# Kernel tuning notes

Measured on AMD Instinct MI355X. Metric: run time of the kernel, lower is better.

Reference implementation:

```python
import jax, jax.numpy as jnp
import numpy as np
from jax import lax


def _pairwise_dist(a, b):
    # a: (T, D), b: (T, D) -> (T, T) Euclidean distances via GEMM trick
    a2 = jnp.sum(a * a, axis=-1)
    b2 = jnp.sum(b * b, axis=-1)
    sq = a2[:, None] + b2[None, :] - 2.0 * (a @ b.T)
    return jnp.sqrt(jnp.maximum(sq, 1e-12))


def _frechet(seq1, seq2):
    cost = _pairwise_dist(seq1, seq2)  # (T, T)
    ca0 = lax.cummax(cost[0])          # first row boundary: running max

    def row_step(prev, cost_row):
        # prev: ca[i-1, :]; cost_row: cost[i, :]
        c0 = jnp.maximum(prev[0], cost_row[0])  # first-column boundary

        def col_step(left, x):
            c, up, diag = x
            val = jnp.maximum(c, jnp.minimum(jnp.minimum(up, left), diag))
            return val, val

        _, rest = lax.scan(col_step, c0, (cost_row[1:], prev[1:], prev[:-1]))
        cur = jnp.concatenate([c0[None], rest])
        return cur, None

    final_row, _ = lax.scan(row_step, ca0, cost[1:])
    return final_row[-1]


def setup_inputs() -> dict:
    key = jax.random.key(0)
    k1, k2 = jax.random.split(key)
    B, T, D = 32, 1024, 64
    pred = jax.random.normal(k1, (B, T, D), dtype=jnp.float32)
    targ = jax.random.normal(k2, (B, T, D), dtype=jnp.float32)
    return {"pred": pred, "targ": targ}


def reference(pred, targ):
    dists = jax.vmap(_frechet)(pred, targ)  # (B,)
    return jnp.mean(dists)
```

## Files before the change

kernel.cpp:

```cpp
#include <hip/hip_runtime.h>
#include <hip/hip_bf16.h>

#define T_LEN 1024
#define D_DIM 64
#define BATCH 32

__global__ __launch_bounds__(256) void cost_kernel(const float* __restrict__ pred,
                                                   const float* __restrict__ targ,
                                                   float* __restrict__ cost) {
    const int b = blockIdx.z;
    const float* P = pred + (size_t)b * T_LEN * D_DIM;
    const float* T = targ + (size_t)b * T_LEN * D_DIM;
    float* C = cost + (size_t)b * T_LEN * T_LEN;
    const int row0 = blockIdx.y * 64;
    const int col0 = blockIdx.x * 64;

    __shared__ __align__(16) float ps[64][68];
    __shared__ __align__(16) float ts[64][68];
    __shared__ float p2[64], t2[64];

    const int tid = threadIdx.x;

#pragma unroll
    for (int it = 0; it < 4; it++) {
        int f = tid + 256 * it;
        int row = f >> 4;
        int kc = f & 15;
        float4 v = *(const float4*)(P + (size_t)(row0 + row) * D_DIM + 4 * kc);
        ps[4 * kc + 0][row] = v.x; ps[4 * kc + 1][row] = v.y;
        ps[4 * kc + 2][row] = v.z; ps[4 * kc + 3][row] = v.w;
        float4 w = *(const float4*)(T + (size_t)(col0 + row) * D_DIM + 4 * kc);
        ts[4 * kc + 0][row] = w.x; ts[4 * kc + 1][row] = w.y;
        ts[4 * kc + 2][row] = w.z; ts[4 * kc + 3][row] = w.w;
    }
    __syncthreads();

    if (tid < 128) {
        int idx = tid & 63;
        float s = 0.0f;
        if (tid < 64) {
#pragma unroll
            for (int k = 0; k < 64; k++) { float x = ps[k][idx]; s += x * x; }
            p2[idx] = s;
        } else {
#pragma unroll
            for (int k = 0; k < 64; k++) { float x = ts[k][idx]; s += x * x; }
            t2[idx] = s;
        }
    }
    __syncthreads();

    const int tx = tid & 15, ty = tid >> 4;
    const int r0 = 4 * ty, c0 = 4 * tx;
    float acc[4][4];
#pragma unroll
    for (int i = 0; i < 4; i++)
#pragma unroll
        for (int j = 0; j < 4; j++) acc[i][j] = 0.0f;

#pragma unroll 8
    for (int k = 0; k < 64; k++) {
        float4 a = *(const float4*)&ps[k][r0];
        float4 bb = *(const float4*)&ts[k][c0];
        float av[4] = {a.x, a.y, a.z, a.w};
        float bv[4] = {bb.x, bb.y, bb.z, bb.w};
#pragma unroll
        for (int i = 0; i < 4; i++)
#pragma unroll
            for (int j = 0; j < 4; j++) acc[i][j] += av[i] * bv[j];
    }

#pragma unroll
    for (int i = 0; i < 4; i++) {
        float4 o;
        float pa = p2[r0 + i];
        float d0 = pa + t2[c0 + 0] - 2.0f * acc[i][0];
        float d1 = pa + t2[c0 + 1] - 2.0f * acc[i][1];
        float d2 = pa + t2[c0 + 2] - 2.0f * acc[i][2];
        float d3 = pa + t2[c0 + 3] - 2.0f * acc[i][3];
        o.x = sqrtf(fmaxf(d0, 1e-12f));
        o.y = sqrtf(fmaxf(d1, 1e-12f));
        o.z = sqrtf(fmaxf(d2, 1e-12f));
        o.w = sqrtf(fmaxf(d3, 1e-12f));
        *(float4*)(C + (size_t)(row0 + r0 + i) * T_LEN + (col0 + c0)) = o;
    }
}

#define PD 8
__global__ __launch_bounds__(64) void dp_kernel(const float* __restrict__ cost,
                                                float* __restrict__ out) {
    const int b = blockIdx.x;
    const int t = threadIdx.x;
    const float INF = __builtin_inff();
    const float* C = cost + (size_t)b * T_LEN * T_LEN + 16 * t;

    float prev[16];
#pragma unroll
    for (int j = 0; j < 16; j++) prev[j] = INF;
    float right_out = INF;
    float diag_feed = INF;

    float4 pipe[PD][4];
#pragma unroll
    for (int d = 0; d < PD; d++) {
        int r = d - t; r = r < 0 ? 0 : (r > T_LEN - 1 ? T_LEN - 1 : r);
        const float4* p = (const float4*)(C + (size_t)r * T_LEN);
        pipe[d][0] = p[0]; pipe[d][1] = p[1]; pipe[d][2] = p[2]; pipe[d][3] = p[3];
    }

    const int S = T_LEN + 63;
    const int NCH = (S + PD - 1) / PD;
    int s = 0;
    for (int chunk = 0; chunk < NCH; chunk++) {
#pragma unroll
        for (int u = 0; u < PD; u++, s++) {
            int r = s - t;
            float inc = __shfl_up(right_out, 1, 64);
            float left = inc, diag = diag_feed;
            diag_feed = inc;
            if (t == 0) { left = (r == 0) ? -INF : INF; diag = INF; }
            if (r >= 0 && r < T_LEN) {
                const float* cb = (const float*)&pipe[u][0];
#pragma unroll
                for (int j = 0; j < 16; j++) {
                    float c = cb[j];
                    float up = prev[j];
                    float v = fmaxf(c, fminf(fminf(up, diag), left));
                    diag = up; left = v; prev[j] = v;
                }
                right_out = left;
            }
            int rn = s + PD - t; rn = rn < 0 ? 0 : (rn > T_LEN - 1 ? T_LEN - 1 : rn);
            const float4* p = (const float4*)(C + (size_t)rn * T_LEN);
            pipe[u][0] = p[0]; pipe[u][1] = p[1]; pipe[u][2] = p[2]; pipe[u][3] = p[3];
        }
    }
    if (t == 63) atomicAdd(out, prev[15] * (1.0f / (float)BATCH));
}

__global__ __launch_bounds__(64) void dp_fused_kernel(const float* __restrict__ pred,
                                                      const float* __restrict__ targ,
                                                      float* __restrict__ out) {
    const int b = blockIdx.x;
    const int t = threadIdx.x;
    const float INF = __builtin_inff();
    const float* P = pred + (size_t)b * T_LEN * D_DIM;
    const float* T = targ + (size_t)b * T_LEN * D_DIM + (size_t)(16 * t) * D_DIM;

    float prev[16];
#pragma unroll
    for (int j = 0; j < 16; j++) prev[j] = INF;
    float right_out = INF;
    float diag_feed = INF;

    for (int s = 0; s < T_LEN + 63; s++) {
        int r = s - t;
        float inc = __shfl_up(right_out, 1, 64);
        float left = inc, diag = diag_feed;
        diag_feed = inc;
        if (t == 0) { left = (r == 0) ? -INF : INF; diag = INF; }
        if (r >= 0 && r < T_LEN) {
            float4 pr[16];
            const float4* pp = (const float4*)(P + (size_t)r * D_DIM);
#pragma unroll
            for (int q = 0; q < 16; q++) pr[q] = pp[q];
#pragma unroll
            for (int j = 0; j < 16; j++) {
                const float4* tp = (const float4*)(T + (size_t)j * D_DIM);
                float acc = 0.0f;
#pragma unroll
                for (int q = 0; q < 16; q++) {
                    float4 tv = tp[q];
                    float dx = pr[q].x - tv.x; acc += dx * dx;
                    float dy = pr[q].y - tv.y; acc += dy * dy;
                    float dz = pr[q].z - tv.z; acc += dz * dz;
                    float dw = pr[q].w - tv.w; acc += dw * dw;
                }
                float c = sqrtf(fmaxf(acc, 1e-12f));
                float up = prev[j];
                float v = fmaxf(c, fminf(fminf(up, diag), left));
                diag = up; left = v; prev[j] = v;
            }
            right_out = left;
        }
    }
    if (t == 63) atomicAdd(out, prev[15] * (1.0f / (float)BATCH));
}

extern "C" void kernel_launch(void* const* d_in, const int* in_sizes, int n_in,
                              void* d_out, int out_size, void* d_ws, size_t ws_size,
                              hipStream_t stream) {
    const float* pred = (const float*)d_in[0];
    const float* targ = (const float*)d_in[1];
    float* out = (float*)d_out;

    hipMemsetAsync(out, 0, sizeof(float) * out_size, stream);

    const size_t per_batch = (size_t)T_LEN * T_LEN * sizeof(float);
    int bpg = (int)(ws_size / per_batch);
    if (bpg > BATCH) bpg = BATCH;

    if (bpg >= 1) {
        float* cost = (float*)d_ws;
        for (int g0 = 0; g0 < BATCH; g0 += bpg) {
            int gb = (BATCH - g0) < bpg ? (BATCH - g0) : bpg;
            dim3 grid(16, 16, gb);
            cost_kernel<<<grid, 256, 0, stream>>>(pred + (size_t)g0 * T_LEN * D_DIM,
                                                  targ + (size_t)g0 * T_LEN * D_DIM,
                                                  cost);
            dp_kernel<<<gb, 64, 0, stream>>>(cost, out);
        }
    } else {
        dp_fused_kernel<<<BATCH, 64, 0, stream>>>(pred, targ, out);
    }
}
```

Baseline: 311.6 us.

## Stream DP cost rows through LDS ring via async global_load_lds, retile cost GEMM

The DP kernel now prefetches cost rows with global_load_lds into a 12-deep shared-memory ring instead of a register pipeline. Explicit vmcnt waits keep about eleven rows in flight, which aims to hide global latency on the serial wavefront without spending registers. The cost kernel moves to 64x128 tiles with 8x4 outputs per thread and a non-transposed P tile, to raise arithmetic per shared-memory load. The hand-tuned vmcnt count is fragile if the compiler emits other memory ops, and the write from the ring's own loads back into the same LDS slot relies on ordering.

```diff
diff --git a/kernel.cpp b/kernel.cpp
--- a/kernel.cpp
+++ b/kernel.cpp
@@ -5,88 +5,111 @@
 #define D_DIM 64
 #define BATCH 32
 
-__global__ __launch_bounds__(256) void cost_kernel(const float* __restrict__ pred,
-                                                   const float* __restrict__ targ,
-                                                   float* __restrict__ cost) {
+#define BM 64
+#define BN 128
+
+__global__ __launch_bounds__(256, 3) void cost_kernel(const float* __restrict__ pred,
+                                                      const float* __restrict__ targ,
+                                                      float* __restrict__ cost) {
     const int b = blockIdx.z;
     const float* P = pred + (size_t)b * T_LEN * D_DIM;
-    const float* T = targ + (size_t)b * T_LEN * D_DIM;
+    const float* Tg = targ + (size_t)b * T_LEN * D_DIM;
     float* C = cost + (size_t)b * T_LEN * T_LEN;
-    const int row0 = blockIdx.y * 64;
-    const int col0 = blockIdx.x * 64;
-
-    __shared__ __align__(16) float ps[64][68];
-    __shared__ __align__(16) float ts[64][68];
-    __shared__ float p2[64], t2[64];
+    const int row0 = blockIdx.y * BM;
+    const int col0 = blockIdx.x * BN;
+
+    __shared__ __align__(16) float ps[BM][D_DIM + 4];
+    __shared__ __align__(16) float ts[D_DIM][BN + 4];
+    __shared__ float p2[BM], t2[BN];
 
     const int tid = threadIdx.x;
 
 #pragma unroll
-    for (int it = 0; it < 4; it++) {
+    for (int it = 0; it < 4; ++it) {
         int f = tid + 256 * it;
         int row = f >> 4;
         int kc = f & 15;
         float4 v = *(const float4*)(P + (size_t)(row0 + row) * D_DIM + 4 * kc);
-        ps[4 * kc + 0][row] = v.x; ps[4 * kc + 1][row] = v.y;
-        ps[4 * kc + 2][row] = v.z; ps[4 * kc + 3][row] = v.w;
-        float4 w = *(const float4*)(T + (size_t)(col0 + row) * D_DIM + 4 * kc);
-        ts[4 * kc + 0][row] = w.x; ts[4 * kc + 1][row] = w.y;
-        ts[4 * kc + 2][row] = w.z; ts[4 * kc + 3][row] = w.w;
+        *(float4*)&ps[row][4 * kc] = v;
+    }
+#pragma unroll
+    for (int it = 0; it < 8; ++it) {
+        int f = tid + 256 * it;
+        int col = f >> 4;
+        int kc = f & 15;
+        float4 w = *(const float4*)(Tg + (size_t)(col0 + col) * D_DIM + 4 * kc);
+        ts[4 * kc + 0][col] = w.x;
+        ts[4 * kc + 1][col] = w.y;
+        ts[4 * kc + 2][col] = w.z;
+        ts[4 * kc + 3][col] = w.w;
     }
     __syncthreads();
 
-    if (tid < 128) {
-        int idx = tid & 63;
+    if (tid < 64) {
         float s = 0.0f;
-        if (tid < 64) {
-#pragma unroll
-            for (int k = 0; k < 64; k++) { float x = ps[k][idx]; s += x * x; }
-            p2[idx] = s;
-        } else {
-#pragma unroll
-            for (int k = 0; k < 64; k++) { float x = ts[k][idx]; s += x * x; }
-            t2[idx] = s;
-        }
+        const float4* pr = (const float4*)&ps[tid][0];
+#pragma unroll
+        for (int q = 0; q < 16; ++q) {
+            float4 v = pr[q];
+            s += v.x * v.x; s += v.y * v.y; s += v.z * v.z; s += v.w * v.w;
+        }
+        p2[tid] = s;
+    } else if (tid < 192) {
+        int c = tid - 64;
+        float s = 0.0f;
+#pragma unroll
+        for (int k = 0; k < 64; ++k) { float x = ts[k][c]; s += x * x; }
+        t2[c] = s;
     }
     __syncthreads();
 
-    const int tx = tid & 15, ty = tid >> 4;
-    const int r0 = 4 * ty, c0 = 4 * tx;
-    float acc[4][4];
-#pragma unroll
-    for (int i = 0; i < 4; i++)
-#pragma unroll
-        for (int j = 0; j < 4; j++) acc[i][j] = 0.0f;
-
-#pragma unroll 8
-    for (int k = 0; k < 64; k++) {
-        float4 a = *(const float4*)&ps[k][r0];
-        float4 bb = *(const float4*)&ts[k][c0];
-        float av[4] = {a.x, a.y, a.z, a.w};
-        float bv[4] = {bb.x, bb.y, bb.z, bb.w};
-#pragma unroll
-        for (int i = 0; i < 4; i++)
-#pragma unroll
-            for (int j = 0; j < 4; j++) acc[i][j] += av[i] * bv[j];
-    }
-
-#pragma unroll
-    for (int i = 0; i < 4; i++) {
+    const int tx = tid & 31;
+    const int ty = tid >> 5;
+    const int r0 = 8 * ty, c0 = 4 * tx;
+
+    float acc[8][4];
+#pragma unroll
+    for (int i = 0; i < 8; ++i)
+#pragma unroll
+        for (int j = 0; j < 4; ++j) acc[i][j] = 0.0f;
+
+#pragma unroll
+    for (int k4 = 0; k4 < 16; ++k4) {
+        float4 b0 = *(const float4*)&ts[4 * k4 + 0][c0];
+        float4 b1 = *(const float4*)&ts[4 * k4 + 1][c0];
+        float4 b2 = *(const float4*)&ts[4 * k4 + 2][c0];
+        float4 b3 = *(const float4*)&ts[4 * k4 + 3][c0];
+#pragma unroll
+        for (int i = 0; i < 8; ++i) {
+            float4 a = *(const float4*)&ps[r0 + i][4 * k4];
+            acc[i][0] += a.x * b0.x; acc[i][1] += a.x * b0.y; acc[i][2] += a.x * b0.z; acc[i][3] += a.x * b0.w;
+            acc[i][0] += a.y * b1.x; acc[i][1] += a.y * b1.y; acc[i][2] += a.y * b1.z; acc[i][3] += a.y * b1.w;
+            acc[i][0] += a.z * b2.x; acc[i][1] += a.z * b2.y; acc[i][2] += a.z * b2.z; acc[i][3] += a.z * b2.w;
+            acc[i][0] += a.w * b3.x; acc[i][1] += a.w * b3.y; acc[i][2] += a.w * b3.z; acc[i][3] += a.w * b3.w;
+        }
+    }
+
+    float4 tt = *(const float4*)&t2[c0];
+#pragma unroll
+    for (int i = 0; i < 8; ++i) {
+        float pa = p2[r0 + i];
         float4 o;
-        float pa = p2[r0 + i];
-        float d0 = pa + t2[c0 + 0] - 2.0f * acc[i][0];
-        float d1 = pa + t2[c0 + 1] - 2.0f * acc[i][1];
-        float d2 = pa + t2[c0 + 2] - 2.0f * acc[i][2];
-        float d3 = pa + t2[c0 + 3] - 2.0f * acc[i][3];
-        o.x = sqrtf(fmaxf(d0, 1e-12f));
-        o.y = sqrtf(fmaxf(d1, 1e-12f));
-        o.z = sqrtf(fmaxf(d2, 1e-12f));
-        o.w = sqrtf(fmaxf(d3, 1e-12f));
+        o.x = sqrtf(fmaxf(pa + tt.x - 2.0f * acc[i][0], 1e-12f));
+        o.y = sqrtf(fmaxf(pa + tt.y - 2.0f * acc[i][1], 1e-12f));
+        o.z = sqrtf(fmaxf(pa + tt.z - 2.0f * acc[i][2], 1e-12f));
+        o.w = sqrtf(fmaxf(pa + tt.w - 2.0f * acc[i][3], 1e-12f));
         *(float4*)(C + (size_t)(row0 + r0 + i) * T_LEN + (col0 + c0)) = o;
     }
 }
 
-#define PD 8
+#define RD 12
+
+__device__ __forceinline__ void gl_lds16(const float* g, void* l) {
+    __builtin_amdgcn_global_load_lds(
+        (const __attribute__((address_space(1))) unsigned int*)(const void*)g,
+        (__attribute__((address_space(3))) unsigned int*)l, 16, 0, 0);
+}
+
 __global__ __launch_bounds__(64) void dp_kernel(const float* __restrict__ cost,
                                                 float* __restrict__ out) {
     const int b = blockIdx.x;
@@ -94,35 +117,45 @@
     const float INF = __builtin_inff();
     const float* C = cost + (size_t)b * T_LEN * T_LEN + 16 * t;
 
+    __shared__ __align__(16) float4 ring[RD][4][64];
+
     float prev[16];
 #pragma unroll
-    for (int j = 0; j < 16; j++) prev[j] = INF;
+    for (int j = 0; j < 16; ++j) prev[j] = INF;
     float right_out = INF;
     float diag_feed = INF;
 
-    float4 pipe[PD][4];
-#pragma unroll
-    for (int d = 0; d < PD; d++) {
+#pragma unroll
+    for (int d = 0; d < RD; ++d) {
         int r = d - t; r = r < 0 ? 0 : (r > T_LEN - 1 ? T_LEN - 1 : r);
-        const float4* p = (const float4*)(C + (size_t)r * T_LEN);
-        pipe[d][0] = p[0]; pipe[d][1] = p[1]; pipe[d][2] = p[2]; pipe[d][3] = p[3];
+        const float* src = C + (size_t)r * T_LEN;
+#pragma unroll
+        for (int q = 0; q < 4; ++q) gl_lds16(src + 4 * q, &ring[d][q][0]);
     }
 
     const int S = T_LEN + 63;
-    const int NCH = (S + PD - 1) / PD;
+    const int NCH = (S + RD - 1) / RD;
     int s = 0;
-    for (int chunk = 0; chunk < NCH; chunk++) {
-#pragma unroll
-        for (int u = 0; u < PD; u++, s++) {
+    for (int chunk = 0; chunk < NCH; ++chunk) {
+#pragma unroll
+        for (int u = 0; u < RD; ++u, ++s) {
+            asm volatile("s_waitcnt vmcnt(44)" ::: "memory");
+            __builtin_amdgcn_sched_barrier(0);
+            float4 c0 = ring[u][0][t];
+            float4 c1 = ring[u][1][t];
+            float4 c2 = ring[u][2][t];
+            float4 c3 = ring[u][3][t];
+
             int r = s - t;
             float inc = __shfl_up(right_out, 1, 64);
             float left = inc, diag = diag_feed;
             diag_feed = inc;
             if (t == 0) { left = (r == 0) ? -INF : INF; diag = INF; }
             if (r >= 0 && r < T_LEN) {
-                const float* cb = (const float*)&pipe[u][0];
-#pragma unroll
-                for (int j = 0; j < 16; j++) {
+                float cb[16] = {c0.x, c0.y, c0.z, c0.w, c1.x, c1.y, c1.z, c1.w,
+                                c2.x, c2.y, c2.z, c2.w, c3.x, c3.y, c3.z, c3.w};
+#pragma unroll
+                for (int j = 0; j < 16; ++j) {
                     float c = cb[j];
                     float up = prev[j];
                     float v = fmaxf(c, fminf(fminf(up, diag), left));
@@ -130,11 +163,15 @@
                 }
                 right_out = left;
             }
-            int rn = s + PD - t; rn = rn < 0 ? 0 : (rn > T_LEN - 1 ? T_LEN - 1 : rn);
-            const float4* p = (const float4*)(C + (size_t)rn * T_LEN);
-            pipe[u][0] = p[0]; pipe[u][1] = p[1]; pipe[u][2] = p[2]; pipe[u][3] = p[3];
-        }
-    }
+            {
+                int rn = s + RD - t; rn = rn < 0 ? 0 : (rn > T_LEN - 1 ? T_LEN - 1 : rn);
+                const float* src = C + (size_t)rn * T_LEN;
+#pragma unroll
+                for (int q = 0; q < 4; ++q) gl_lds16(src + 4 * q, &ring[u][q][0]);
+            }
+        }
+    }
+    asm volatile("s_waitcnt vmcnt(0)" ::: "memory");
     if (t == 63) atomicAdd(out, prev[15] * (1.0f / (float)BATCH));
 }
 
@@ -149,7 +186,7 @@
 
     float prev[16];
 #pragma unroll
-    for (int j = 0; j < 16; j++) prev[j] = INF;
+    for (int j = 0; j < 16; ++j) prev[j] = INF;
     float right_out = INF;
     float diag_feed = INF;
 
@@ -204,7 +241,7 @@
         float* cost = (float*)d_ws;
         for (int g0 = 0; g0 < BATCH; g0 += bpg) {
             int gb = (BATCH - g0) < bpg ? (BATCH - g0) : bpg;
-            dim3 grid(16, 16, gb);
+            dim3 grid(T_LEN / BN, T_LEN / BM, gb);
             cost_kernel<<<grid, 256, 0, stream>>>(pred + (size_t)g0 * T_LEN * D_DIM,
                                                   targ + (size_t)g0 * T_LEN * D_DIM,
                                                   cost);
```

Result: slower. 659.2 us (+111.6%).
